# Optimization experiments

Measured on AMD Instinct MI355X. Metric: run time of the kernel, lower is better.

Reference implementation:

```python
import jax, jax.numpy as jnp
import numpy as np

N_EMBD = 2048
N_HEAD = 32
HEAD_SIZE = 64          # n_embd // n_head
MIX_DIM = 64            # RWKV-6 time-mix LoRA dim
DECAY_DIM = 128         # RWKV-6 decay LoRA dim
BATCH = 1024
STATE_ROWS = (2 + HEAD_SIZE) * 1  # single block, i = 0


def setup_inputs() -> dict:
    key = jax.random.key(0)
    ks = jax.random.split(key, 32)
    rn = lambda k, shp, s=0.02: jax.random.normal(k, shp, jnp.float32) * s
    d = {}
    d['x'] = jax.random.normal(ks[0], (BATCH, N_EMBD), jnp.float32)
    d['state'] = jax.random.normal(ks[1], (BATCH, STATE_ROWS, N_EMBD), jnp.float32) * 0.1
    d['ln1_w'] = jnp.ones((N_EMBD,), jnp.float32)
    d['ln1_b'] = jnp.zeros((N_EMBD,), jnp.float32)
    d['ln2_w'] = jnp.ones((N_EMBD,), jnp.float32)
    d['ln2_b'] = jnp.zeros((N_EMBD,), jnp.float32)
    d['maa_x'] = rn(ks[2], (N_EMBD,), 0.1)
    d['maa_w'] = rn(ks[3], (N_EMBD,), 0.1)
    d['maa_k'] = rn(ks[4], (N_EMBD,), 0.1)
    d['maa_v'] = rn(ks[5], (N_EMBD,), 0.1)
    d['maa_r'] = rn(ks[6], (N_EMBD,), 0.1)
    d['maa_g'] = rn(ks[7], (N_EMBD,), 0.1)
    d['maa_w1'] = rn(ks[8], (N_EMBD, 5 * MIX_DIM))
    d['maa_w2'] = rn(ks[9], (5, MIX_DIM, N_EMBD))
    d['decay'] = rn(ks[10], (N_EMBD,), 0.5) - 4.0  # typical negative log-decay
    d['decay_w1'] = rn(ks[11], (N_EMBD, DECAY_DIM))
    d['decay_w2'] = rn(ks[12], (DECAY_DIM, N_EMBD))
    d['faaaa'] = rn(ks[13], (N_HEAD, HEAD_SIZE, 1), 0.1)
    d['Wr'] = rn(ks[14], (N_EMBD, N_EMBD))
    d['Wk'] = rn(ks[15], (N_EMBD, N_EMBD))
    d['Wv'] = rn(ks[16], (N_EMBD, N_EMBD))
    d['Wo'] = rn(ks[17], (N_EMBD, N_EMBD))
    d['Wg'] = rn(ks[18], (N_EMBD, N_EMBD))
    d['gn_w'] = jnp.ones((N_EMBD,), jnp.float32)
    d['gn_b'] = jnp.zeros((N_EMBD,), jnp.float32)
    d['ffn_maa_k'] = rn(ks[19], (N_EMBD,), 0.1)
    d['ffn_maa_r'] = rn(ks[20], (N_EMBD,), 0.1)
    d['ffn_Wk'] = rn(ks[21], (N_EMBD, N_EMBD))
    d['ffn_Wr'] = rn(ks[22], (N_EMBD, N_EMBD))
    d['ffn_Wv'] = rn(ks[23], (N_EMBD, N_EMBD))
    d['i'] = 0
    return d


def _ln(x, w, b):
    mu = jnp.mean(x, -1, keepdims=True)
    var = jnp.var(x, -1, keepdims=True)
    return (x - mu) * jax.lax.rsqrt(var + 1e-5) * w + b


def reference(x, state, ln1_w, ln1_b, ln2_w, ln2_b,
              maa_x, maa_w, maa_k, maa_v, maa_r, maa_g, maa_w1, maa_w2,
              decay, decay_w1, decay_w2, faaaa,
              Wr, Wk, Wv, Wo, Wg, gn_w, gn_b,
              ffn_maa_k, ffn_maa_r, ffn_Wk, ffn_Wr, ffn_Wv, i):
    B = x.shape[0]
    H, S = N_HEAD, HEAD_SIZE
    # ---------------- time mixing ----------------
    xn = _ln(x, ln1_w, ln1_b)
    i1 = (2 + S) * i + 1
    sx = state[:, i1] - xn                                  # token shift delta
    xxx = xn + sx * maa_x
    xxx = jnp.tanh(xxx @ maa_w1).reshape(B, 5, 1, MIX_DIM)
    xxx = jnp.matmul(xxx, maa_w2).reshape(B, 5, N_EMBD)     # [B,5,E]
    mw, mk, mv, mr, mg = (xxx[:, j] for j in range(5))
    xw = xn + sx * (maa_w + mw)
    xk = xn + sx * (maa_k + mk)
    xv = xn + sx * (maa_v + mv)
    xr = xn + sx * (maa_r + mr)
    xg = xn + sx * (maa_g + mg)
    w = decay + jnp.tanh(xw @ decay_w1) @ decay_w2          # [B,E]
    w = jnp.exp(-jnp.exp(w.reshape(B, H, S, 1)))            # decay gate
    r = (xr @ Wr.T).reshape(B, H, 1, S)
    k = (xk @ Wk.T).reshape(B, H, S, 1)
    v = (xv @ Wv.T).reshape(B, H, 1, S)
    g = jax.nn.silu(xg @ Wg.T)
    s = state[:, (2 + S) * i + 2:(2 + S) * (i + 1), :].reshape(B, H, S, S)
    a = jnp.matmul(k, v)                                    # [B,H,S,S] outer product
    y = jnp.matmul(r, faaaa * a + s).reshape(B, N_EMBD)     # wkv readout
    # group norm (n_head groups over n_embd channels)
    yg = y.reshape(B, H, S)
    mu = jnp.mean(yg, -1, keepdims=True)
    var = jnp.var(yg, -1, keepdims=True)
    yg = ((yg - mu) * jax.lax.rsqrt(var + 1e-5)).reshape(B, N_EMBD) * gn_w + gn_b
    x1 = x + (yg * g) @ Wo.T
    # ---------------- channel mixing ----------------
    xn2 = _ln(x1, ln2_w, ln2_b)
    i0 = (2 + S) * i
    sx2 = state[:, i0] - xn2
    xk2 = xn2 + sx2 * ffn_maa_k
    xr2 = xn2 + sx2 * ffn_maa_r
    rr = jax.nn.sigmoid(xr2 @ ffn_Wr.T)
    kk = jnp.square(jax.nn.relu(xk2 @ ffn_Wk.T))
    return x1 + rr * (kk @ ffn_Wv.T)
```

## Files before the change

kernel.cpp:

```cpp
#include <hip/hip_runtime.h>
#include <cstdint>
#include <cstddef>

typedef unsigned short u16;
typedef __attribute__((ext_vector_type(8))) short bf16x8;
typedef __attribute__((ext_vector_type(4))) float f32x4;

#define DEV __device__ __forceinline__

DEV u16 f2bf(float f) {
  uint32_t b = __float_as_uint(f);
  b += 0x7fffu + ((b >> 16) & 1u);
  return (u16)(b >> 16);
}
DEV float bf2f(u16 u) { return __uint_as_float(((uint32_t)u) << 16); }

DEV void gl16(const u16* g, u16* l) {
  __builtin_amdgcn_global_load_lds(
      (const __attribute__((address_space(1))) void*)g,
      (__attribute__((address_space(3))) void*)l, 16, 0, 0);
}

struct CvtArgs { const float* s[8]; };

__global__ __launch_bounds__(256) void k_cvt_ln(
    const float* __restrict__ w1, const float* __restrict__ w2,
    u16* __restrict__ w1t, u16* __restrict__ w2t,
    const float* __restrict__ x, const float* __restrict__ state,
    const int* __restrict__ ip,
    const float* __restrict__ lw, const float* __restrict__ lb,
    const float* __restrict__ mx,
    u16* __restrict__ xn_o, u16* __restrict__ sx_o, u16* __restrict__ a1_o) {
  __shared__ float ls1[4], ls2[4];
  if (blockIdx.x < 4608) {
    int idx = blockIdx.x * 256 + threadIdx.x;
    if (idx < 655360) {
      int n = idx >> 11, k = idx & 2047;
      w1t[idx] = f2bf(w1[(size_t)k * 320 + n]);
    } else {
      int r = idx - 655360;
      int j = r >> 17, q = r & 131071;
      int n = q >> 6, k2 = q & 63;
      w2t[r] = f2bf(w2[((size_t)(j + 1) * 64 + k2) * 2048 + n]);
    }
  } else {
    int b = blockIdx.x - 4608, t = threadIdx.x;
    const float* xr = x + (size_t)b * 2048;
    float4 v0 = *(const float4*)(xr + t * 8);
    float4 v1 = *(const float4*)(xr + t * 8 + 4);
    float xv[8] = {v0.x, v0.y, v0.z, v0.w, v1.x, v1.y, v1.z, v1.w};
    float s1 = 0.f, s2 = 0.f;
#pragma unroll
    for (int j = 0; j < 8; ++j) { s1 += xv[j]; s2 += xv[j] * xv[j]; }
#pragma unroll
    for (int off = 32; off; off >>= 1) { s1 += __shfl_xor(s1, off); s2 += __shfl_xor(s2, off); }
    int w = t >> 6;
    if ((t & 63) == 0) { ls1[w] = s1; ls2[w] = s2; }
    __syncthreads();
    s1 = ls1[0] + ls1[1] + ls1[2] + ls1[3];
    s2 = ls2[0] + ls2[1] + ls2[2] + ls2[3];
    float mu = s1 * (1.0f / 2048.0f);
    float var = s2 * (1.0f / 2048.0f) - mu * mu;
    float rs = rsqrtf(var + 1e-5f);
    const float* st = state + ((size_t)b * 66 + (size_t)66 * ip[0] + 1) * 2048;
    int e0 = t * 8;
    uint4 xnp, sxp, a1p;
    u16* xnl = (u16*)&xnp; u16* sxl = (u16*)&sxp; u16* a1l = (u16*)&a1p;
#pragma unroll
    for (int j = 0; j < 8; ++j) {
      int e = e0 + j;
      float xn = (xv[j] - mu) * rs * lw[e] + lb[e];
      float sxv = st[e] - xn;
      xnl[j] = f2bf(xn); sxl[j] = f2bf(sxv); a1l[j] = f2bf(xn + sxv * mx[e]);
    }
    size_t o = (size_t)b * 2048 + e0;
    *(uint4*)(xn_o + o) = xnp;
    *(uint4*)(sx_o + o) = sxp;
    *(uint4*)(a1_o + o) = a1p;
  }
}

__global__ __launch_bounds__(256) void k_tanhpack(const float* __restrict__ p2,
                                                  u16* __restrict__ xb) {
  int idx = blockIdx.x * 256 + threadIdx.x;
  float s = p2[idx] + p2[327680 + idx] + p2[2 * 327680 + idx] + p2[3 * 327680 + idx];
  xb[idx] = f2bf(tanhf(s));
}

__global__ __launch_bounds__(256) void k_act(const u16* __restrict__ p8,
                                             u16* __restrict__ rr, u16* __restrict__ kk) {
  const size_t S = 2097152;
  int gid = blockIdx.x * 256 + threadIdx.x;
  size_t e0 = (size_t)(gid & 262143) * 8;
  int isk = gid >= 262144;
  const u16* base = p8 + (isk ? 4 * S : 0) + e0;
  float acc[8] = {};
#pragma unroll
  for (int s = 0; s < 4; ++s) {
    uint4 v = *(const uint4*)(base + (size_t)s * S);
    u16* vl = (u16*)&v;
#pragma unroll
    for (int j = 0; j < 8; ++j) acc[j] += bf2f(vl[j]);
  }
  uint4 p; u16* pl = (u16*)&p;
  if (!isk) {
#pragma unroll
    for (int j = 0; j < 8; ++j) pl[j] = f2bf(1.f / (1.f + __expf(-acc[j])));
    *(uint4*)(rr + e0) = p;
  } else {
#pragma unroll
    for (int j = 0; j < 8; ++j) { float r = acc[j] > 0.f ? acc[j] : 0.f; pl[j] = f2bf(r * r); }
    *(uint4*)(kk + e0) = p;
  }
}

__global__ __launch_bounds__(256) void k_fin(const float* __restrict__ x1,
                                             const u16* __restrict__ p9,
                                             const u16* __restrict__ rr,
                                             float* __restrict__ out) {
  const size_t S = 2097152;
  size_t e0 = ((size_t)blockIdx.x * 256 + threadIdx.x) * 8;
  float acc[8] = {};
#pragma unroll
  for (int s = 0; s < 4; ++s) {
    uint4 v = *(const uint4*)(p9 + (size_t)s * S + e0);
    u16* vl = (u16*)&v;
#pragma unroll
    for (int j = 0; j < 8; ++j) acc[j] += bf2f(vl[j]);
  }
  float4 x0 = *(const float4*)(x1 + e0), x4 = *(const float4*)(x1 + e0 + 4);
  float xv[8] = {x0.x, x0.y, x0.z, x0.w, x4.x, x4.y, x4.z, x4.w};
  uint4 rv = *(const uint4*)(rr + e0); u16* rl = (u16*)&rv;
  float o[8];
#pragma unroll
  for (int j = 0; j < 8; ++j) o[j] = xv[j] + bf2f(rl[j]) * acc[j];
  *(float4*)(out + e0) = make_float4(o[0], o[1], o[2], o[3]);
  *(float4*)(out + e0 + 4) = make_float4(o[4], o[5], o[6], o[7]);
}

__global__ __launch_bounds__(256) void k_ln_mix2(
    const float* __restrict__ x, const u16* __restrict__ p6,
    const float* __restrict__ state, const int* __restrict__ ip,
    const float* __restrict__ lw, const float* __restrict__ lb,
    const float* __restrict__ mk, const float* __restrict__ mr,
    u16* __restrict__ xk_o, u16* __restrict__ xr_o, float* __restrict__ x1_o) {
  const size_t S = 2097152;
  int b = blockIdx.x, t = threadIdx.x;
  size_t off = (size_t)b * 2048 + t * 8;
  float4 v0 = *(const float4*)(x + off);
  float4 v1 = *(const float4*)(x + off + 4);
  float xv[8] = {v0.x, v0.y, v0.z, v0.w, v1.x, v1.y, v1.z, v1.w};
#pragma unroll
  for (int s = 0; s < 4; ++s) {
    uint4 v = *(const uint4*)(p6 + (size_t)s * S + off);
    u16* vl = (u16*)&v;
#pragma unroll
    for (int j = 0; j < 8; ++j) xv[j] += bf2f(vl[j]);
  }
  *(float4*)(x1_o + off) = make_float4(xv[0], xv[1], xv[2], xv[3]);
  *(float4*)(x1_o + off + 4) = make_float4(xv[4], xv[5], xv[6], xv[7]);
  float s1 = 0.f, s2 = 0.f;
#pragma unroll
  for (int j = 0; j < 8; ++j) { s1 += xv[j]; s2 += xv[j] * xv[j]; }
#pragma unroll
  for (int off2 = 32; off2; off2 >>= 1) { s1 += __shfl_xor(s1, off2); s2 += __shfl_xor(s2, off2); }
  __shared__ float ls1[4], ls2[4];
  int w = t >> 6;
  if ((t & 63) == 0) { ls1[w] = s1; ls2[w] = s2; }
  __syncthreads();
  s1 = ls1[0] + ls1[1] + ls1[2] + ls1[3];
  s2 = ls2[0] + ls2[1] + ls2[2] + ls2[3];
  float mu = s1 * (1.0f / 2048.0f);
  float var = s2 * (1.0f / 2048.0f) - mu * mu;
  float rs = rsqrtf(var + 1e-5f);
  const float* st = state + ((size_t)b * 66 + (size_t)66 * ip[0] + 0) * 2048;
  int e0 = t * 8;
  uint4 xkp, xrp;
  u16* xkl = (u16*)&xkp; u16* xrl = (u16*)&xrp;
#pragma unroll
  for (int j = 0; j < 8; ++j) {
    int e = e0 + j;
    float xn = (xv[j] - mu) * rs * lw[e] + lb[e];
    float sxv = st[e] - xn;
    xkl[j] = f2bf(xn + sxv * mk[e]);
    xrl[j] = f2bf(xn + sxv * mr[e]);
  }
  *(uint4*)(xk_o + off) = xkp;
  *(uint4*)(xr_o + off) = xrp;
}

enum { EP_STORE = 0, EP_SILU, EP_MIX, EP_STOREF };

struct GemmDesc {
  const u16* A; const u16* B; void* C;
  const void* p1; const void* p2; const float* pvec;
  int lda, ldb, ldc, N, K, k0, ep;
};
struct GemmBatch { GemmDesc g[8]; int bpg; };

__global__ __launch_bounds__(256, 3) void k_gemmc(GemmBatch bat, int ngemm,
                                                  CvtArgs ca, u16* __restrict__ cdst,
                                                  int cvtoff) {
  if (blockIdx.x >= ngemm) {
    size_t idx = ((size_t)(blockIdx.x - ngemm + cvtoff) * 256 + threadIdx.x) * 8;
    int w = (int)(idx >> 22);
    size_t off = idx & ((1u << 22) - 1);
    const float* s = ca.s[w];
    float4 v0 = *(const float4*)(s + off);
    float4 v1 = *(const float4*)(s + off + 4);
    uint4 p; u16* pl = (u16*)&p;
    pl[0] = f2bf(v0.x); pl[1] = f2bf(v0.y); pl[2] = f2bf(v0.z); pl[3] = f2bf(v0.w);
    pl[4] = f2bf(v1.x); pl[5] = f2bf(v1.y); pl[6] = f2bf(v1.z); pl[7] = f2bf(v1.w);
    *(uint4*)(cdst + ((size_t)w << 22) + off) = p;
    return;
  }
  int gi = blockIdx.x / bat.bpg;
  int bid = blockIdx.x % bat.bpg;
  GemmDesc g = bat.g[gi];
  int ntn = (g.N + 127) >> 7;
  int m0 = (bid / ntn) << 7;
  int n0 = (bid % ntn) << 7;
  __shared__ u16 As[2][128 * 32];
  __shared__ u16 Bs[2][128 * 32];
  int t = threadIdx.x, w = t >> 6, lane = t & 63;
  int wm = w >> 1, wn = w & 1;
  int lr = lane & 15, kb = (lane >> 4) * 8;
  const u16* Ab = g.A + (size_t)(m0 + w * 32 + (lane >> 2)) * g.lda + (lane & 3) * 8;
  const u16* Bb = g.B + (size_t)(n0 + w * 32 + (lane >> 2)) * g.ldb + (lane & 3) * 8;
  int a16 = 16 * g.lda, b16 = 16 * g.ldb;
  int aoff = (w * 32) * 32;
  f32x4 acc[4][4] = {};
  int nt = g.K >> 5;

  auto stage = [&](int buf, int kk) {
    u16* Ad = (u16*)As + buf * 4096 + aoff;
    u16* Bd = (u16*)Bs + buf * 4096 + aoff;
    gl16(Ab + kk, Ad);
    gl16(Ab + kk + a16, Ad + 512);
    gl16(Bb + kk, Bd);
    gl16(Bb + kk + b16, Bd + 512);
  };

  stage(0, g.k0);
  __syncthreads();
  int cur = 0;
  for (int ti = 0; ti < nt; ++ti) {
    if (ti + 1 < nt) stage(cur ^ 1, g.k0 + (ti + 1) * 32);
    const u16* Ac = (const u16*)As + cur * 4096;
    const u16* Bc = (const u16*)Bs + cur * 4096;
    bf16x8 af[4], bfr[4];
#pragma unroll
    for (int m = 0; m < 4; ++m)
      af[m] = *(const bf16x8*)(Ac + (wm * 64 + m * 16 + lr) * 32 + kb);
#pragma unroll
    for (int n = 0; n < 4; ++n)
      bfr[n] = *(const bf16x8*)(Bc + (wn * 64 + n * 16 + lr) * 32 + kb);
#pragma unroll
    for (int m = 0; m < 4; ++m)
#pragma unroll
      for (int n = 0; n < 4; ++n)
        acc[m][n] = __builtin_amdgcn_mfma_f32_16x16x32_bf16(af[m], bfr[n], acc[m][n], 0, 0, 0);
    __syncthreads();
    cur ^= 1;
  }

  int ep = g.ep;
#pragma unroll
  for (int m = 0; m < 4; ++m) {
    int grow0 = m0 + wm * 64 + m * 16 + (lane >> 4) * 4;
#pragma unroll
    for (int n = 0; n < 4; ++n) {
      int gc = n0 + wn * 64 + n * 16 + lr;
      if (gc >= g.N) continue;
#pragma unroll
      for (int q = 0; q < 4; ++q) {
        size_t ci = (size_t)(grow0 + q) * g.ldc + gc;
        float v = acc[m][n][q];
        switch (ep) {
          case EP_STORE: ((u16*)g.C)[ci] = f2bf(v); break;
          case EP_MIX: {
            float xn = bf2f(((const u16*)g.p1)[ci]);
            float sxv = bf2f(((const u16*)g.p2)[ci]);
            ((u16*)g.C)[ci] = f2bf(xn + sxv * (g.pvec[gc] + v));
          } break;
          case EP_STOREF: ((float*)g.C)[ci] = v; break;
          default: break;
        }
      }
    }
  }
}

__global__ __launch_bounds__(512, 2) void k_gemm2(GemmBatch bat) {
  extern __shared__ u16 lds[];
  int nwg = gridDim.x;
  int wg0 = blockIdx.x;
  int wg = (wg0 & 7) * (nwg >> 3) + (wg0 >> 3);
  int gi = wg / bat.bpg;
  int bid = wg % bat.bpg;
  GemmDesc g = bat.g[gi];
  int ntn = (g.N + 255) >> 8;
  int m0 = (bid / ntn) << 7;
  int n0 = (bid % ntn) << 8;
  int t = threadIdx.x, wv = t >> 6, lane = t & 63;
  int wm = wv >> 2, wn = wv & 3;
  int lr = lane & 15, hi = lane >> 4;

  const u16* asrc[2]; const u16* bsrc[4];
#pragma unroll
  for (int j = 0; j < 2; ++j) {
    int cid = t + 512 * j, r = cid >> 3, c = cid & 7;
    asrc[j] = g.A + (size_t)(m0 + r) * g.lda + ((c ^ (r & 7)) << 3);
  }
#pragma unroll
  for (int j = 0; j < 4; ++j) {
    int cid = t + 512 * j, r = cid >> 3, c = cid & 7;
    bsrc[j] = g.B + (size_t)(n0 + r) * g.ldb + ((c ^ (r & 7)) << 3);
  }
  int au = wv * 512;

  auto stage = [&](int buf, int k) {
    u16* base = lds + buf * 24576;
#pragma unroll
    for (int j = 0; j < 2; ++j) gl16(asrc[j] + k, base + au + j * 4096);
#pragma unroll
    for (int j = 0; j < 4; ++j) gl16(bsrc[j] + k, base + 8192 + au + j * 4096);
  };

  int arow[4], brow[4];
#pragma unroll
  for (int m = 0; m < 4; ++m) arow[m] = wm * 64 + m * 16 + lr;
#pragma unroll
  for (int n = 0; n < 4; ++n) brow[n] = wn * 64 + n * 16 + lr;

  f32x4 acc[4][4] = {};
  int nt = g.K >> 6;
  stage(0, g.k0);
  if (nt > 1) stage(1, g.k0 + 64);

  for (int ti = 0; ti < nt; ++ti) {
    if (ti + 1 < nt) asm volatile("s_waitcnt vmcnt(6)" ::: "memory");
    else             asm volatile("s_waitcnt vmcnt(0)" ::: "memory");
    __builtin_amdgcn_sched_barrier(0);
    __builtin_amdgcn_s_barrier();
    __builtin_amdgcn_sched_barrier(0);
    const u16* buf = lds + (ti % 3) * 24576;
    bf16x8 af[4][2], bf[4][2];
#pragma unroll
    for (int m = 0; m < 4; ++m)
#pragma unroll
      for (int ks = 0; ks < 2; ++ks)
        af[m][ks] = *(const bf16x8*)(buf + arow[m] * 64 + ((((ks << 2) + hi) ^ (arow[m] & 7)) << 3));
#pragma unroll
    for (int n = 0; n < 4; ++n)
#pragma unroll
      for (int ks = 0; ks < 2; ++ks)
        bf[n][ks] = *(const bf16x8*)(buf + 8192 + brow[n] * 64 + ((((ks << 2) + hi) ^ (brow[n] & 7)) << 3));
    if (ti + 2 < nt) stage((ti + 2) % 3, g.k0 + (ti + 2) * 64);
    __builtin_amdgcn_s_setprio(1);
#pragma unroll
    for (int m = 0; m < 4; ++m)
#pragma unroll
      for (int n = 0; n < 4; ++n)
#pragma unroll
        for (int ks = 0; ks < 2; ++ks)
          acc[m][n] = __builtin_amdgcn_mfma_f32_16x16x32_bf16(af[m][ks], bf[n][ks], acc[m][n], 0, 0, 0);
    __builtin_amdgcn_s_setprio(0);
  }

  int ep = g.ep;
#pragma unroll
  for (int m = 0; m < 4; ++m) {
    int grow0 = m0 + wm * 64 + m * 16 + hi * 4;
#pragma unroll
    for (int n = 0; n < 4; ++n) {
      int gc = n0 + wn * 64 + n * 16 + lr;
#pragma unroll
      for (int q = 0; q < 4; ++q) {
        size_t ci = (size_t)(grow0 + q) * g.ldc + gc;
        float v = acc[m][n][q];
        switch (ep) {
          case EP_STORE: ((u16*)g.C)[ci] = f2bf(v); break;
          case EP_SILU:  ((u16*)g.C)[ci] = f2bf(v / (1.f + __expf(-v))); break;
          case EP_STOREF: ((float*)g.C)[ci] = v; break;
          default: break;
        }
      }
    }
  }
}

__global__ __launch_bounds__(512, 2) void k_gemm3(GemmBatch bat) {
  extern __shared__ u16 lds[];
  int nwg = gridDim.x;
  int wg0 = blockIdx.x;
  int wg = (wg0 & 7) * (nwg >> 3) + (wg0 >> 3);
  GemmDesc g = bat.g[wg / bat.bpg];
  int bid = wg % bat.bpg;
  int ntn = g.N >> 8;
  int m0 = (bid / ntn) << 8;
  int n0 = (bid % ntn) << 8;
  int t = threadIdx.x, wv = t >> 6, lane = t & 63;
  int wm = wv >> 2, wn = wv & 3;
  int lr = lane & 15, hi = lane >> 4;

  const u16* asrc[4]; const u16* bsrc[4];
#pragma unroll
  for (int j = 0; j < 4; ++j) {
    int cid = t + 512 * j, r = cid >> 3, c = cid & 7;
    asrc[j] = g.A + (size_t)(m0 + r) * g.lda + ((c ^ (r & 7)) << 3);
    bsrc[j] = g.B + (size_t)(n0 + r) * g.ldb + ((c ^ (r & 7)) << 3);
  }
  int au = wv * 512;

  auto stage = [&](int buf, int k) {
    u16* ab = lds + buf * 32768 + au;
    u16* bb = lds + buf * 32768 + 16384 + au;
#pragma unroll
    for (int j = 0; j < 4; ++j) gl16(asrc[j] + k, ab + j * 4096);
#pragma unroll
    for (int j = 0; j < 4; ++j) gl16(bsrc[j] + k, bb + j * 4096);
  };

  int arow[8], brow[4];
#pragma unroll
  for (int m = 0; m < 8; ++m) arow[m] = wm * 128 + m * 16 + lr;
#pragma unroll
  for (int n = 0; n < 4; ++n) brow[n] = wn * 64 + n * 16 + lr;

  f32x4 acc[8][4] = {};
  int nt = g.K >> 6;
  stage(0, g.k0);
  if (nt > 1) stage(1, g.k0 + 64);

  for (int ti = 0; ti < nt; ++ti) {
    if (ti + 1 < nt) asm volatile("s_waitcnt vmcnt(8)" ::: "memory");
    else             asm volatile("s_waitcnt vmcnt(0)" ::: "memory");
    __builtin_amdgcn_sched_barrier(0);
    __builtin_amdgcn_s_barrier();
    __builtin_amdgcn_sched_barrier(0);
    const u16* buf = lds + (ti & 1) * 32768;
#pragma unroll
    for (int ks = 0; ks < 2; ++ks) {
      bf16x8 af[8], bf[4];
#pragma unroll
      for (int m = 0; m < 8; ++m)
        af[m] = *(const bf16x8*)(buf + arow[m] * 64 + ((((ks << 2) + hi) ^ (arow[m] & 7)) << 3));
#pragma unroll
      for (int n = 0; n < 4; ++n)
        bf[n] = *(const bf16x8*)(buf + 16384 + brow[n] * 64 + ((((ks << 2) + hi) ^ (brow[n] & 7)) << 3));
      __builtin_amdgcn_s_setprio(1);
#pragma unroll
      for (int m = 0; m < 8; ++m)
#pragma unroll
        for (int n = 0; n < 4; ++n)
          acc[m][n] = __builtin_amdgcn_mfma_f32_16x16x32_bf16(af[m], bf[n], acc[m][n], 0, 0, 0);
      __builtin_amdgcn_s_setprio(0);
    }
    __builtin_amdgcn_sched_barrier(0);
    __builtin_amdgcn_s_barrier();
    __builtin_amdgcn_sched_barrier(0);
    if (ti + 2 < nt) stage(ti & 1, g.k0 + (ti + 2) * 64);
  }

#pragma unroll
  for (int m = 0; m < 8; ++m) {
    int grow0 = m0 + wm * 128 + m * 16 + hi * 4;
#pragma unroll
    for (int n = 0; n < 4; ++n) {
      int gc = n0 + wn * 64 + n * 16 + lr;
#pragma unroll
      for (int q = 0; q < 4; ++q)
        ((u16*)g.C)[(size_t)(grow0 + q) * g.ldc + gc] = f2bf(acc[m][n][q]);
    }
  }
}

__global__ __launch_bounds__(256) void k_wkv(
    const u16* __restrict__ p4,
    const float* __restrict__ state, const int* __restrict__ ip,
    const float* __restrict__ fa, const float* __restrict__ gw,
    const float* __restrict__ gbias, u16* __restrict__ t_o) {
  const size_t S = 2097152;
  int t = threadIdx.x, w = t >> 6, lane = t & 63;
  int flat = blockIdx.x * 4 + w;
  int b = flat >> 5, h = flat & 31;
  size_t base = ((size_t)b << 11) + (h << 6) + lane;
  float r  = bf2f(p4[base])         + bf2f(p4[S + base]);
  float kv = bf2f(p4[2 * S + base]) + bf2f(p4[3 * S + base]);
  float vv = bf2f(p4[4 * S + base]) + bf2f(p4[5 * S + base]);
  float gs = bf2f(p4[6 * S + base]) + bf2f(p4[7 * S + base]);
  float gg = gs / (1.f + __expf(-gs));
  float f  = fa[(h << 6) + lane];
  __shared__ float rs[4][64];
  rs[w][lane] = r;
  __syncthreads();
  float c = r * f * kv;
#pragma unroll
  for (int off = 32; off; off >>= 1) c += __shfl_xor(c, off);

  const float* sp = state + ((size_t)b * 66 + (size_t)66 * ip[0] + 2 + 2 * h) * 2048;
  int q = lane >> 4, jj = lane & 15;
  float yp0 = 0.f, yp1 = 0.f, yp2 = 0.f, yp3 = 0.f;
#pragma unroll
  for (int ib = 0; ib < 16; ++ib) {
    int i = ib * 4 + q;
    float4 sv = *(const float4*)(sp + ((i >> 5) * 2048) + ((i & 31) << 6) + jj * 4);
    float ri = rs[w][i];
    yp0 += ri * sv.x; yp1 += ri * sv.y; yp2 += ri * sv.z; yp3 += ri * sv.w;
  }
#pragma unroll
  for (int off = 16; off <= 32; off <<= 1) {
    yp0 += __shfl_xor(yp0, off); yp1 += __shfl_xor(yp1, off);
    yp2 += __shfl_xor(yp2, off); yp3 += __shfl_xor(yp3, off);
  }
  int src = lane >> 2, cc = lane & 3;
  float t0 = __shfl(yp0, src), t1 = __shfl(yp1, src);
  float t2 = __shfl(yp2, src), t3 = __shfl(yp3, src);
  float y = cc == 0 ? t0 : cc == 1 ? t1 : cc == 2 ? t2 : t3;
  y += c * vv;
  float s1 = y, s2 = y * y;
#pragma unroll
  for (int off = 32; off; off >>= 1) { s1 += __shfl_xor(s1, off); s2 += __shfl_xor(s2, off); }
  float mu = s1 * (1.f / 64.f);
  float var = s2 * (1.f / 64.f) - mu * mu;
  float yn = (y - mu) * rsqrtf(var + 1e-5f);
  float tg = (yn * gw[(h << 6) + lane] + gbias[(h << 6) + lane]) * gg;
  t_o[((size_t)b << 11) + (h << 6) + lane] = f2bf(tg);
}

extern "C" void kernel_launch(void* const* d_in, const int* in_sizes, int n_in,
                              void* d_out, int out_size, void* d_ws, size_t ws_size,
                              hipStream_t stream) {
  const float* x      = (const float*)d_in[0];
  const float* state  = (const float*)d_in[1];
  const float* ln1_w  = (const float*)d_in[2];
  const float* ln1_b  = (const float*)d_in[3];
  const float* ln2_w  = (const float*)d_in[4];
  const float* ln2_b  = (const float*)d_in[5];
  const float* maa_x  = (const float*)d_in[6];
  const float* maa_k  = (const float*)d_in[8];
  const float* maa_v  = (const float*)d_in[9];
  const float* maa_r  = (const float*)d_in[10];
  const float* maa_g  = (const float*)d_in[11];
  const float* maa_w1 = (const float*)d_in[12];
  const float* maa_w2 = (const float*)d_in[13];
  const float* faaaa  = (const float*)d_in[17];
  const float* Wr     = (const float*)d_in[18];
  const float* Wk     = (const float*)d_in[19];
  const float* Wv     = (const float*)d_in[20];
  const float* Wo     = (const float*)d_in[21];
  const float* Wg     = (const float*)d_in[22];
  const float* gn_w   = (const float*)d_in[23];
  const float* gn_b   = (const float*)d_in[24];
  const float* fmk    = (const float*)d_in[25];
  const float* fmr    = (const float*)d_in[26];
  const float* fWk    = (const float*)d_in[27];
  const float* fWr    = (const float*)d_in[28];
  const float* fWv    = (const float*)d_in[29];
  const int*   ip     = (const int*)d_in[30];
  float* out = (float*)d_out;

  char* wsb = (char*)d_ws;
  const size_t MB = 1ull << 20;
  u16* wbf   = (u16*)(wsb + 0 * MB);
  u16* w1t   = (u16*)(wsb + 64 * MB);
  u16* w2t   = (u16*)(wsb + 66 * MB);
  u16* xn    = (u16*)(wsb + 68 * MB);
  u16* sx    = (u16*)(wsb + 72 * MB);
  u16* a1    = (u16*)(wsb + 76 * MB);
  float* p2  = (float*)(wsb + 80 * MB);
  u16* xxx   = (u16*)(wsb + 86 * MB);
  u16* xk    = (u16*)(wsb + 87 * MB);
  u16* xv    = (u16*)(wsb + 91 * MB);
  u16* xr    = (u16*)(wsb + 95 * MB);
  u16* xg    = (u16*)(wsb + 99 * MB);
  u16* p4    = (u16*)(wsb + 103 * MB);
  u16* tb    = (u16*)(wsb + 135 * MB);
  u16* p6    = (u16*)(wsb + 139 * MB);
  float* x1  = (float*)(wsb + 155 * MB);
  u16* xk2   = (u16*)(wsb + 163 * MB);
  u16* xr2   = (u16*)(wsb + 167 * MB);
  u16* p8    = (u16*)(wsb + 171 * MB);
  u16* rr    = (u16*)(wsb + 203 * MB);
  u16* kkb   = (u16*)(wsb + 207 * MB);
  u16* p9    = (u16*)(wsb + 211 * MB);

  const size_t WSQ = 4194304, S = 2097152;
  u16* bWr = wbf + 0 * WSQ; u16* bWk = wbf + 1 * WSQ; u16* bWv = wbf + 2 * WSQ;
  u16* bWg = wbf + 3 * WSQ; u16* bWo = wbf + 4 * WSQ; u16* bfWr = wbf + 5 * WSQ;
  u16* bfWk = wbf + 6 * WSQ; u16* bfWv = wbf + 7 * WSQ;

  auto mkd = [](const u16* A, const u16* B, void* C, const void* p1,
                const void* p2_, const float* pvec, int lda, int ldb, int ldc,
                int N, int K, int k0, int epf) {
    GemmDesc d; d.A = A; d.B = B; d.C = C; d.p1 = p1; d.p2 = p2_; d.pvec = pvec;
    d.lda = lda; d.ldb = ldb; d.ldc = ldc; d.N = N; d.K = K; d.k0 = k0; d.ep = epf;
    return d;
  };

  CvtArgs ca; ca.s[0] = Wr; ca.s[1] = Wk; ca.s[2] = Wv; ca.s[3] = Wg;
  ca.s[4] = Wo; ca.s[5] = fWr; ca.s[6] = fWk; ca.s[7] = fWv;

  static const int LDS2 = 147456;
  static const int LDS3 = 131072;
  hipFuncSetAttribute((const void*)k_gemm2,
                      hipFuncAttributeMaxDynamicSharedMemorySize, LDS2);
  hipFuncSetAttribute((const void*)k_gemm3,
                      hipFuncAttributeMaxDynamicSharedMemorySize, LDS3);

  k_cvt_ln<<<5632, 256, 0, stream>>>(maa_w1, maa_w2, w1t, w2t,
                                     x, state, ip, ln1_w, ln1_b, maa_x, xn, sx, a1);

  {
    GemmBatch g{}; g.bpg = 8 * 3;
    for (int j = 0; j < 4; ++j)
      g.g[j] = mkd(a1, w1t, p2 + (size_t)j * 327680, nullptr, nullptr, nullptr,
                   2048, 2048, 320, 320, 512, j * 512, EP_STOREF);
    k_gemmc<<<96 + 8192, 256, 0, stream>>>(g, 96, ca, wbf, 0);
  }
  k_tanhpack<<<1280, 256, 0, stream>>>(p2, xxx);

  {
    GemmBatch g{}; g.bpg = 8 * 16;
    const float* mv[4] = {maa_k, maa_v, maa_r, maa_g};
    u16* tv[4] = {xk, xv, xr, xg};
    for (int j = 1; j <= 4; ++j)
      g.g[j - 1] = mkd(xxx + j * 64, w2t + (size_t)(j - 1) * 131072, tv[j - 1],
                       xn, sx, mv[j - 1], 320, 64, 2048, 2048, 64, 0, EP_MIX);
    k_gemmc<<<512 + 8192, 256, 0, stream>>>(g, 512, ca, wbf, 8192);
  }

  {
    GemmBatch g{}; g.bpg = 32;
    const u16* av[4] = {xr, xk, xv, xg};
    const u16* bv[4] = {bWr, bWk, bWv, bWg};
    for (int q = 0; q < 4; ++q)
      for (int s = 0; s < 2; ++s)
        g.g[q * 2 + s] = mkd(av[q], bv[q], p4 + (size_t)(q * 2 + s) * S,
                             nullptr, nullptr, nullptr, 2048, 2048, 2048,
                             2048, 1024, s * 1024, EP_STORE);
    k_gemm3<<<256, 512, LDS3, stream>>>(g);
  }

  k_wkv<<<8192, 256, 0, stream>>>(p4, state, ip, faaaa, gn_w, gn_b, tb);

  {
    GemmBatch g{}; g.bpg = 8 * 8;
    for (int s = 0; s < 4; ++s)
      g.g[s] = mkd(tb, bWo, p6 + (size_t)s * S, nullptr, nullptr, nullptr,
                   2048, 2048, 2048, 2048, 512, s * 512, EP_STORE);
    k_gemm2<<<256, 512, LDS2, stream>>>(g);
  }

  k_ln_mix2<<<1024, 256, 0, stream>>>(x, p6, state, ip, ln2_w, ln2_b, fmk, fmr,
                                      xk2, xr2, x1);

  {
    GemmBatch g{}; g.bpg = 32;
    for (int s = 0; s < 4; ++s) {
      g.g[s]     = mkd(xr2, bfWr, p8 + (size_t)s * S, nullptr, nullptr, nullptr,
                       2048, 2048, 2048, 2048, 512, s * 512, EP_STORE);
      g.g[4 + s] = mkd(xk2, bfWk, p8 + (size_t)(4 + s) * S, nullptr, nullptr, nullptr,
                       2048, 2048, 2048, 2048, 512, s * 512, EP_STORE);
    }
    k_gemm3<<<256, 512, LDS3, stream>>>(g);
  }
  k_act<<<2048, 256, 0, stream>>>(p8, rr, kkb);

  {
    GemmBatch g{}; g.bpg = 8 * 8;
    for (int s = 0; s < 4; ++s)
      g.g[s] = mkd(kkb, bfWv, p9 + (size_t)s * S, nullptr, nullptr, nullptr,
                   2048, 2048, 2048, 2048, 512, s * 512, EP_STORE);
    k_gemm2<<<256, 512, LDS2, stream>>>(g);
  }

  k_fin<<<1024, 256, 0, stream>>>(x1, p9, rr, out);
}
```

Measured before the change: 320.2 us.

## Overlap WKV state readout with K/V/G GEMM in a mixed-role kernel

The R projection is split out into its own GEMM launch. The K, V and G projections then run in a combined kernel whose extra blocks compute the memory-bound r·state dot product into a float buffer. The aim is to hide the large state read behind the MFMA-bound GEMM work. The cost is an extra GEMM launch, a split-K of 4 for R, an extra float buffer round trip, and interleaved block scheduling that could disturb GEMM occupancy.

After: 340.9 us. 1.06x slower.

```diff
diff --git a/kernel.cpp b/kernel.cpp
--- a/kernel.cpp
+++ b/kernel.cpp
@@ -476,9 +476,128 @@
   }
 }
 
-__global__ __launch_bounds__(256) void k_wkv(
-    const u16* __restrict__ p4,
-    const float* __restrict__ state, const int* __restrict__ ip,
+__global__ __launch_bounds__(512, 2) void k_kvg_wkv(GemmBatch bat,
+    const u16* __restrict__ pr, const float* __restrict__ state,
+    const int* __restrict__ ip, float* __restrict__ ydot) {
+  extern __shared__ u16 lds[];
+  const size_t S = 2097152;
+  int gid = blockIdx.x;
+  int w67 = gid / 67, r67 = gid % 67;
+  if (r67 >= 3) {
+    int dot_idx = w67 * 64 + (r67 - 3);
+    int t = threadIdx.x, wv = t >> 6, lane = t & 63;
+    int flat = dot_idx * 8 + wv;
+    int b = flat >> 5, h = flat & 31;
+    size_t rbase = ((size_t)b << 11) + (h << 6);
+    float rv = bf2f(pr[rbase + lane]) + bf2f(pr[S + rbase + lane]) +
+               bf2f(pr[2 * S + rbase + lane]) + bf2f(pr[3 * S + rbase + lane]);
+    const float* sp = state + ((size_t)b * 66 + (size_t)66 * ip[0] + 2 + 2 * h) * 2048;
+    int q = lane >> 4, jj = lane & 15;
+    float yp0 = 0.f, yp1 = 0.f, yp2 = 0.f, yp3 = 0.f;
+#pragma unroll
+    for (int ib = 0; ib < 16; ++ib) {
+      int i = ib * 4 + q;
+      float4 sv = *(const float4*)(sp + ((i >> 5) * 2048) + ((i & 31) << 6) + jj * 4);
+      float ri = __shfl(rv, i);
+      yp0 += ri * sv.x; yp1 += ri * sv.y; yp2 += ri * sv.z; yp3 += ri * sv.w;
+    }
+#pragma unroll
+    for (int off = 16; off <= 32; off <<= 1) {
+      yp0 += __shfl_xor(yp0, off); yp1 += __shfl_xor(yp1, off);
+      yp2 += __shfl_xor(yp2, off); yp3 += __shfl_xor(yp3, off);
+    }
+    int src = lane >> 2, cc2 = lane & 3;
+    float t0 = __shfl(yp0, src), t1 = __shfl(yp1, src);
+    float t2 = __shfl(yp2, src), t3 = __shfl(yp3, src);
+    float y = cc2 == 0 ? t0 : cc2 == 1 ? t1 : cc2 == 2 ? t2 : t3;
+    ydot[rbase + lane] = y;
+    return;
+  }
+  int wg = w67 * 3 + r67;
+  GemmDesc g = bat.g[wg / bat.bpg];
+  int bid = wg % bat.bpg;
+  int ntn = g.N >> 8;
+  int m0 = (bid / ntn) << 8;
+  int n0 = (bid % ntn) << 8;
+  int t = threadIdx.x, wv = t >> 6, lane = t & 63;
+  int wm = wv >> 2, wn = wv & 3;
+  int lr = lane & 15, hi = lane >> 4;
+
+  const u16* asrc[4]; const u16* bsrc[4];
+#pragma unroll
+  for (int j = 0; j < 4; ++j) {
+    int cid = t + 512 * j, r = cid >> 3, c = cid & 7;
+    asrc[j] = g.A + (size_t)(m0 + r) * g.lda + ((c ^ (r & 7)) << 3);
+    bsrc[j] = g.B + (size_t)(n0 + r) * g.ldb + ((c ^ (r & 7)) << 3);
+  }
+  int au = wv * 512;
+
+  auto stage = [&](int buf, int k) {
+    u16* ab = lds + buf * 32768 + au;
+    u16* bb = lds + buf * 32768 + 16384 + au;
+#pragma unroll
+    for (int j = 0; j < 4; ++j) gl16(asrc[j] + k, ab + j * 4096);
+#pragma unroll
+    for (int j = 0; j < 4; ++j) gl16(bsrc[j] + k, bb + j * 4096);
+  };
+
+  int arow[8], brow[4];
+#pragma unroll
+  for (int m = 0; m < 8; ++m) arow[m] = wm * 128 + m * 16 + lr;
+#pragma unroll
+  for (int n = 0; n < 4; ++n) brow[n] = wn * 64 + n * 16 + lr;
+
+  f32x4 acc[8][4] = {};
+  int nt = g.K >> 6;
+  stage(0, g.k0);
+  if (nt > 1) stage(1, g.k0 + 64);
+
+  for (int ti = 0; ti < nt; ++ti) {
+    if (ti + 1 < nt) asm volatile("s_waitcnt vmcnt(8)" ::: "memory");
+    else             asm volatile("s_waitcnt vmcnt(0)" ::: "memory");
+    __builtin_amdgcn_sched_barrier(0);
+    __builtin_amdgcn_s_barrier();
+    __builtin_amdgcn_sched_barrier(0);
+    const u16* buf = lds + (ti & 1) * 32768;
+#pragma unroll
+    for (int ks = 0; ks < 2; ++ks) {
+      bf16x8 af[8], bf[4];
+#pragma unroll
+      for (int m = 0; m < 8; ++m)
+        af[m] = *(const bf16x8*)(buf + arow[m] * 64 + ((((ks << 2) + hi) ^ (arow[m] & 7)) << 3));
+#pragma unroll
+      for (int n = 0; n < 4; ++n)
+        bf[n] = *(const bf16x8*)(buf + 16384 + brow[n] * 64 + ((((ks << 2) + hi) ^ (brow[n] & 7)) << 3));
+      __builtin_amdgcn_s_setprio(1);
+#pragma unroll
+      for (int m = 0; m < 8; ++m)
+#pragma unroll
+        for (int n = 0; n < 4; ++n)
+          acc[m][n] = __builtin_amdgcn_mfma_f32_16x16x32_bf16(af[m], bf[n], acc[m][n], 0, 0, 0);
+      __builtin_amdgcn_s_setprio(0);
+    }
+    __builtin_amdgcn_sched_barrier(0);
+    __builtin_amdgcn_s_barrier();
+    __builtin_amdgcn_sched_barrier(0);
+    if (ti + 2 < nt) stage(ti & 1, g.k0 + (ti + 2) * 64);
+  }
+
+#pragma unroll
+  for (int m = 0; m < 8; ++m) {
+    int grow0 = m0 + wm * 128 + m * 16 + hi * 4;
+#pragma unroll
+    for (int n = 0; n < 4; ++n) {
+      int gc = n0 + wn * 64 + n * 16 + lr;
+#pragma unroll
+      for (int q = 0; q < 4; ++q)
+        ((u16*)g.C)[(size_t)(grow0 + q) * g.ldc + gc] = f2bf(acc[m][n][q]);
+    }
+  }
+}
+
+__global__ __launch_bounds__(256) void k_wkv_fin(
+    const u16* __restrict__ pr, const u16* __restrict__ p4,
+    const float* __restrict__ ydot,
     const float* __restrict__ fa, const float* __restrict__ gw,
     const float* __restrict__ gbias, u16* __restrict__ t_o) {
   const size_t S = 2097152;
@@ -486,39 +605,17 @@
   int flat = blockIdx.x * 4 + w;
   int b = flat >> 5, h = flat & 31;
   size_t base = ((size_t)b << 11) + (h << 6) + lane;
-  float r  = bf2f(p4[base])         + bf2f(p4[S + base]);
-  float kv = bf2f(p4[2 * S + base]) + bf2f(p4[3 * S + base]);
-  float vv = bf2f(p4[4 * S + base]) + bf2f(p4[5 * S + base]);
-  float gs = bf2f(p4[6 * S + base]) + bf2f(p4[7 * S + base]);
+  float r  = bf2f(pr[base]) + bf2f(pr[S + base]) +
+             bf2f(pr[2 * S + base]) + bf2f(pr[3 * S + base]);
+  float kv = bf2f(p4[base])         + bf2f(p4[S + base]);
+  float vv = bf2f(p4[2 * S + base]) + bf2f(p4[3 * S + base]);
+  float gs = bf2f(p4[4 * S + base]) + bf2f(p4[5 * S + base]);
   float gg = gs / (1.f + __expf(-gs));
   float f  = fa[(h << 6) + lane];
-  __shared__ float rs[4][64];
-  rs[w][lane] = r;
-  __syncthreads();
   float c = r * f * kv;
 #pragma unroll
   for (int off = 32; off; off >>= 1) c += __shfl_xor(c, off);
-
-  const float* sp = state + ((size_t)b * 66 + (size_t)66 * ip[0] + 2 + 2 * h) * 2048;
-  int q = lane >> 4, jj = lane & 15;
-  float yp0 = 0.f, yp1 = 0.f, yp2 = 0.f, yp3 = 0.f;
-#pragma unroll
-  for (int ib = 0; ib < 16; ++ib) {
-    int i = ib * 4 + q;
-    float4 sv = *(const float4*)(sp + ((i >> 5) * 2048) + ((i & 31) << 6) + jj * 4);
-    float ri = rs[w][i];
-    yp0 += ri * sv.x; yp1 += ri * sv.y; yp2 += ri * sv.z; yp3 += ri * sv.w;
-  }
-#pragma unroll
-  for (int off = 16; off <= 32; off <<= 1) {
-    yp0 += __shfl_xor(yp0, off); yp1 += __shfl_xor(yp1, off);
-    yp2 += __shfl_xor(yp2, off); yp3 += __shfl_xor(yp3, off);
-  }
-  int src = lane >> 2, cc = lane & 3;
-  float t0 = __shfl(yp0, src), t1 = __shfl(yp1, src);
-  float t2 = __shfl(yp2, src), t3 = __shfl(yp3, src);
-  float y = cc == 0 ? t0 : cc == 1 ? t1 : cc == 2 ? t2 : t3;
-  y += c * vv;
+  float y = ydot[base] + c * vv;
   float s1 = y, s2 = y * y;
 #pragma unroll
   for (int off = 32; off; off >>= 1) { s1 += __shfl_xor(s1, off); s2 += __shfl_xor(s2, off); }
@@ -526,7 +623,7 @@
   float var = s2 * (1.f / 64.f) - mu * mu;
   float yn = (y - mu) * rsqrtf(var + 1e-5f);
   float tg = (yn * gw[(h << 6) + lane] + gbias[(h << 6) + lane]) * gg;
-  t_o[((size_t)b << 11) + (h << 6) + lane] = f2bf(tg);
+  t_o[base] = f2bf(tg);
 }
 
 extern "C" void kernel_launch(void* const* d_in, const int* in_sizes, int n_in,
@@ -575,16 +672,18 @@
   u16* xv    = (u16*)(wsb + 91 * MB);
   u16* xr    = (u16*)(wsb + 95 * MB);
   u16* xg    = (u16*)(wsb + 99 * MB);
-  u16* p4    = (u16*)(wsb + 103 * MB);
-  u16* tb    = (u16*)(wsb + 135 * MB);
-  u16* p6    = (u16*)(wsb + 139 * MB);
-  float* x1  = (float*)(wsb + 155 * MB);
-  u16* xk2   = (u16*)(wsb + 163 * MB);
-  u16* xr2   = (u16*)(wsb + 167 * MB);
-  u16* p8    = (u16*)(wsb + 171 * MB);
-  u16* rr    = (u16*)(wsb + 203 * MB);
-  u16* kkb   = (u16*)(wsb + 207 * MB);
-  u16* p9    = (u16*)(wsb + 211 * MB);
+  u16* pr    = (u16*)(wsb + 103 * MB);
+  u16* p4    = (u16*)(wsb + 119 * MB);
+  float* ydot = (float*)(wsb + 143 * MB);
+  u16* tb    = (u16*)(wsb + 151 * MB);
+  u16* p6    = (u16*)(wsb + 155 * MB);
+  float* x1  = (float*)(wsb + 171 * MB);
+  u16* xk2   = (u16*)(wsb + 179 * MB);
+  u16* xr2   = (u16*)(wsb + 183 * MB);
+  u16* p8    = (u16*)(wsb + 187 * MB);
+  u16* rr    = (u16*)(wsb + 219 * MB);
+  u16* kkb   = (u16*)(wsb + 223 * MB);
+  u16* p9    = (u16*)(wsb + 227 * MB);
 
   const size_t WSQ = 4194304, S = 2097152;
   u16* bWr = wbf + 0 * WSQ; u16* bWk = wbf + 1 * WSQ; u16* bWv = wbf + 2 * WSQ;
@@ -607,6 +706,8 @@
   hipFuncSetAttribute((const void*)k_gemm2,
                       hipFuncAttributeMaxDynamicSharedMemorySize, LDS2);
   hipFuncSetAttribute((const void*)k_gemm3,
+                      hipFuncAttributeMaxDynamicSharedMemorySize, LDS3);
+  hipFuncSetAttribute((const void*)k_kvg_wkv,
                       hipFuncAttributeMaxDynamicSharedMemorySize, LDS3);
 
   k_cvt_ln<<<5632, 256, 0, stream>>>(maa_w1, maa_w2, w1t, w2t,
@@ -632,18 +733,26 @@
   }
 
   {
+    GemmBatch g{}; g.bpg = 8 * 8;
+    for (int s = 0; s < 4; ++s)
+      g.g[s] = mkd(xr, bWr, pr + (size_t)s * S, nullptr, nullptr, nullptr,
+                   2048, 2048, 2048, 2048, 512, s * 512, EP_STORE);
+    k_gemm2<<<256, 512, LDS2, stream>>>(g);
+  }
+
+  {
     GemmBatch g{}; g.bpg = 32;
-    const u16* av[4] = {xr, xk, xv, xg};
-    const u16* bv[4] = {bWr, bWk, bWv, bWg};
-    for (int q = 0; q < 4; ++q)
+    const u16* av[3] = {xk, xv, xg};
+    const u16* bv[3] = {bWk, bWv, bWg};
+    for (int q = 0; q < 3; ++q)
       for (int s = 0; s < 2; ++s)
         g.g[q * 2 + s] = mkd(av[q], bv[q], p4 + (size_t)(q * 2 + s) * S,
                              nullptr, nullptr, nullptr, 2048, 2048, 2048,
                              2048, 1024, s * 1024, EP_STORE);
-    k_gemm3<<<256, 512, LDS3, stream>>>(g);
-  }
-
-  k_wkv<<<8192, 256, 0, stream>>>(p4, state, ip, faaaa, gn_w, gn_b, tb);
+    k_kvg_wkv<<<4288, 512, LDS3, stream>>>(g, pr, state, ip, ydot);
+  }
+
+  k_wkv_fin<<<8192, 256, 0, stream>>>(pr, p4, ydot, faaaa, gn_w, gn_b, tb);
 
   {
     GemmBatch g{}; g.bpg = 8 * 8;
```
